# Kernel tuning notes

Measured on AMD Instinct MI355X. Metric: run time of the kernel, lower is better.

Reference implementation:

```python
import jax, jax.numpy as jnp
import numpy as np

BN_EPS = 1e-5


def setup_inputs() -> dict:
    key = jax.random.key(0)
    ks = jax.random.split(key, 12)
    B, N, S, D1, D2 = 2, 16384, 4096, 128, 256
    C1, C2 = 256, 128  # mlp channels
    return {
        "xyz1": jax.random.normal(ks[0], (B, 3, N), dtype=jnp.float32),
        "xyz2": jax.random.normal(ks[1], (B, 3, S), dtype=jnp.float32),
        "points1": jax.random.normal(ks[2], (B, D1, N), dtype=jnp.float32),
        "points2": jax.random.normal(ks[3], (B, D2, S), dtype=jnp.float32),
        "w1": jax.random.normal(ks[4], (D1 + D2, C1), dtype=jnp.float32) * 0.05,
        "b1": jax.random.normal(ks[5], (C1,), dtype=jnp.float32) * 0.05,
        "g1": jax.random.uniform(ks[6], (C1,), dtype=jnp.float32, minval=0.5, maxval=1.5),
        "beta1": jax.random.normal(ks[7], (C1,), dtype=jnp.float32) * 0.05,
        "w2": jax.random.normal(ks[8], (C1, C2), dtype=jnp.float32) * 0.05,
        "b2": jax.random.normal(ks[9], (C2,), dtype=jnp.float32) * 0.05,
        "g2": jax.random.uniform(ks[10], (C2,), dtype=jnp.float32, minval=0.5, maxval=1.5),
        "beta2": jax.random.normal(ks[11], (C2,), dtype=jnp.float32) * 0.05,
    }


def _conv_bn_relu(x, W, b, g, beta):
    # 1x1 Conv1d == per-point matmul; BatchNorm1d training-mode stats over (B, N).
    y = x @ W + b                              # [B, N, Cout]
    mu = jnp.mean(y, axis=(0, 1))
    var = jnp.var(y, axis=(0, 1))              # biased variance, matches torch BN
    y = g * (y - mu) * jax.lax.rsqrt(var + BN_EPS) + beta
    return jax.nn.relu(y)


def reference(xyz1, xyz2, points1, points2, w1, b1, g1, beta1, w2, b2, g2, beta2):
    x1 = jnp.transpose(xyz1, (0, 2, 1))        # [B, N, 3]
    x2 = jnp.transpose(xyz2, (0, 2, 1))        # [B, S, 3]
    p2 = jnp.transpose(points2, (0, 2, 1))     # [B, S, D2]

    # squared pairwise distance [B, N, S], clamped at 0
    d = (jnp.sum(x1 ** 2, axis=-1, keepdims=True)
         - 2.0 * jnp.einsum('bnc,bsc->bns', x1, x2)
         + jnp.sum(x2 ** 2, axis=-1)[:, None, :])
    d = jnp.maximum(d, 0.0)

    # 3 nearest neighbors (ascending smallest distances) -- same math as full sort + slice
    neg_d3, idx = jax.lax.top_k(-d, 3)         # [B, N, 3]
    d3 = jnp.maximum(-neg_d3, 1e-6)
    recip = 1.0 / d3
    w = recip / jnp.maximum(jnp.sum(recip, axis=-1, keepdims=True), 1e-6)

    nb = jax.vmap(lambda p, i: p[i])(p2, idx)  # [B, N, 3, D2]
    interp = jnp.sum(nb * w[..., None], axis=2)
    interp = jnp.nan_to_num(interp, nan=0.0, posinf=0.0, neginf=0.0)

    p1 = jnp.transpose(points1, (0, 2, 1))     # [B, N, D1]
    x = jnp.concatenate([p1, interp], axis=-1) # [B, N, D1+D2]

    x = _conv_bn_relu(x, w1, b1, g1, beta1)
    x = _conv_bn_relu(x, w2, b2, g2, beta2)
    x = jnp.nan_to_num(x, nan=0.0, posinf=0.0, neginf=0.0)
    return jnp.transpose(x, (0, 2, 1))         # [B, C2, N]
```

## Files before the change

### kernel.cpp

```cpp
#include <hip/hip_runtime.h>

#define B_   2
#define N_   16384
#define S_   4096
#define D1_  128
#define D2_  256
#define C1_  256
#define C2_  128
#define M_   (B_ * N_)

typedef __bf16 bf16_t;
typedef bf16_t bf16x8 __attribute__((ext_vector_type(8)));
typedef float  f32x4  __attribute__((ext_vector_type(4)));

__device__ __forceinline__ void gload16(const void* g, void* l) {
  __builtin_amdgcn_global_load_lds(
      (const __attribute__((address_space(1))) void*)g,
      (__attribute__((address_space(3))) void*)l, 16, 0, 0);
}

#define INSERT3(v, ix)                                                   \
  {                                                                      \
    bool b0_ = (v) < m0, b1_ = (v) < m1, b2_ = (v) < m2;                 \
    float nm0 = fminf((v), m0);                                          \
    float nm1 = fminf(fmaxf((v), m0), m1);                               \
    float nm2 = fminf(fmaxf((v), m1), m2);                               \
    j2 = b1_ ? j1 : (b2_ ? (ix) : j2);                                   \
    j1 = b0_ ? j0 : (b1_ ? (ix) : j1);                                   \
    j0 = b0_ ? (ix) : j0;                                                \
    m0 = nm0; m1 = nm1; m2 = nm2;                                        \
  }

union SMem1 {
  struct { float4 cbuf[1024]; float T3V[2][3][32]; int T3I[2][3][32]; } knn;
  float tile[2][32][33];
};

__global__ __launch_bounds__(512, 8) void phase1_k(const float* __restrict__ xyz1,
                                                   const float* __restrict__ xyz2,
                                                   const float* __restrict__ points1,
                                                   const float* __restrict__ w1,
                                                   const float* __restrict__ w2,
                                                   float* __restrict__ kw,
                                                   int* __restrict__ ki,
                                                   bf16_t* __restrict__ Xp1,
                                                   bf16_t* __restrict__ w1at,
                                                   bf16_t* __restrict__ w2t) {
  __shared__ SMem1 sm;
  int bi = blockIdx.x, t = threadIdx.x;
  if (bi < 1024) {
    int l = t & 63, w = t >> 6;
    int q = l & 31, h = l >> 5;
    int s = w * 2 + h;
    int b  = bi >> 9;
    int nb = (bi & 511) * 32;
    int n  = nb + q;
    const float* X1 = xyz1 + (size_t)b * 3 * N_;
    const float* X2 = xyz2 + (size_t)b * 3 * S_;
    float ax = X1[n], ay = X1[N_ + n], az = X1[2 * N_ + n];
    float p = ax * ax + ay * ay + az * az;
    float m0 = 3e38f, m1 = 3e38f, m2 = 3e38f;
    int   j0 = 0, j1 = 0, j2 = 0;
    for (int r = 0; r < 4; ++r) {
      __syncthreads();
      {
        int i0 = r * 1024 + t;
        float x = X2[i0], y = X2[S_ + i0], z = X2[2 * S_ + i0];
        sm.knn.cbuf[t] = make_float4(-2.f * x, -2.f * y, -2.f * z, x * x + y * y + z * z);
        int i1 = i0 + 512;
        x = X2[i1]; y = X2[S_ + i1]; z = X2[2 * S_ + i1];
        sm.knn.cbuf[t + 512] = make_float4(-2.f * x, -2.f * y, -2.f * z, x * x + y * y + z * z);
      }
      __syncthreads();
      const float4* cs = sm.knn.cbuf + s * 64;
      int base = r * 1024 + s * 64;
#pragma unroll 8
      for (int i = 0; i < 64; ++i) {
        float4 c = cs[i];
        float v = c.w;
        v = fmaf(az, c.z, v);
        v = fmaf(ay, c.y, v);
        v = fmaf(ax, c.x, v);
        int idx = base + i;
        INSERT3(v, idx);
      }
    }
    __syncthreads();
    float* SV = (float*)sm.knn.cbuf;
    int*   SI = (int*)sm.knn.cbuf + 1536;
    SV[(s * 3 + 0) * 32 + q] = m0;  SV[(s * 3 + 1) * 32 + q] = m1;  SV[(s * 3 + 2) * 32 + q] = m2;
    SI[(s * 3 + 0) * 32 + q] = j0;  SI[(s * 3 + 1) * 32 + q] = j1;  SI[(s * 3 + 2) * 32 + q] = j2;
    __syncthreads();
    if (t < 64) {
      int th = t >> 5, tq = t & 31;
      float m0 = 3e38f, m1 = 3e38f, m2 = 3e38f;
      int j0 = 0, j1 = 0, j2 = 0;
      for (int s2 = th * 8; s2 < th * 8 + 8; ++s2)
#pragma unroll
        for (int k = 0; k < 3; ++k) {
          float v = SV[(s2 * 3 + k) * 32 + tq];
          int  ix = SI[(s2 * 3 + k) * 32 + tq];
          INSERT3(v, ix);
        }
      sm.knn.T3V[th][0][tq] = m0; sm.knn.T3V[th][1][tq] = m1; sm.knn.T3V[th][2][tq] = m2;
      sm.knn.T3I[th][0][tq] = j0; sm.knn.T3I[th][1][tq] = j1; sm.knn.T3I[th][2][tq] = j2;
    }
    __syncthreads();
    if (t < 32) {
      float m0 = sm.knn.T3V[0][0][t], m1 = sm.knn.T3V[0][1][t], m2 = sm.knn.T3V[0][2][t];
      int   j0 = sm.knn.T3I[0][0][t], j1 = sm.knn.T3I[0][1][t], j2 = sm.knn.T3I[0][2][t];
#pragma unroll
      for (int k = 0; k < 3; ++k) {
        float v = sm.knn.T3V[1][k][t];
        int  ix = sm.knn.T3I[1][k][t];
        INSERT3(v, ix);
      }
      float d0 = fmaxf(p + m0, 1e-6f);
      float d1 = fmaxf(p + m1, 1e-6f);
      float d2 = fmaxf(p + m2, 1e-6f);
      float r0 = 1.f / d0, r1 = 1.f / d1, r2 = 1.f / d2;
      float dn = fmaxf(r0 + r1 + r2, 1e-6f);
      size_t rr = (size_t)b * N_ + n;
      kw[rr * 3 + 0] = r0 / dn;  kw[rr * 3 + 1] = r1 / dn;  kw[rr * 3 + 2] = r2 / dn;
      ki[rr * 3 + 0] = j0;       ki[rr * 3 + 1] = j1;       ki[rr * 3 + 2] = j2;
    }
  } else if (bi < 3072) {
    int bj = bi - 1024;
    int b = bj >> 10, rest = bj & 1023;
    int n0 = (rest & 255) * 64, c0 = (rest >> 8) * 32;
    int tx = t & 31, ty = (t >> 5) & 7, th = t >> 8;
    const float* src = points1 + (size_t)b * D1_ * N_;
#pragma unroll
    for (int k = 0; k < 4; ++k)
      sm.tile[th][ty + k * 8][tx] = src[(size_t)(c0 + ty + k * 8) * N_ + n0 + th * 32 + tx];
    __syncthreads();
#pragma unroll
    for (int k = 0; k < 4; ++k)
      Xp1[(size_t)(b * N_ + n0 + th * 32 + ty + k * 8) * 128 + c0 + tx] =
          (bf16_t)sm.tile[th][tx][ty + k * 8];
  } else {
    int i = (bi - 3072) * 512 + t;
    if (i < 32768) {
      int n = i >> 7, k = i & 127;
      w1at[i] = (bf16_t)w1[(size_t)k * C1_ + n];
    } else {
      int j = i - 32768;
      int n = j >> 8, k = j & 255;
      w2t[j] = (bf16_t)w2[(size_t)k * C2_ + n];
    }
  }
}

__global__ __launch_bounds__(512) void gemmG_k(const float* __restrict__ points2,
                                               const float* __restrict__ w1,
                                               bf16_t* __restrict__ G) {
  const int LDP = 40;
  __shared__ bf16_t As[128 * LDP];
  __shared__ bf16_t Bs[256 * LDP];
  int t = threadIdx.x, lane = t & 63, w = t >> 6;
  int wr = w >> 2, wc = w & 3;
  int bb = blockIdx.x >> 5;
  int m0 = (blockIdx.x & 31) * 128;
  const float* P2 = points2 + (size_t)bb * D2_ * S_;
  f32x4 acc[4][4];
  f32x4 z = {0.f, 0.f, 0.f, 0.f};
#pragma unroll
  for (int i = 0; i < 4; ++i)
#pragma unroll
    for (int j = 0; j < 4; ++j) acc[i][j] = z;
  int sA = t & 127, kgA = t >> 7;
  int nB = t & 255, kgB = t >> 8;
  for (int k0 = 0; k0 < 256; k0 += 32) {
    __syncthreads();
    {
      bf16x8 ap;
#pragma unroll
      for (int kk = 0; kk < 8; ++kk)
        ap[kk] = (bf16_t)P2[(size_t)(k0 + kgA * 8 + kk) * S_ + m0 + sA];
      *(bf16x8*)&As[sA * LDP + kgA * 8] = ap;
      bf16x8 bp0, bp1;
#pragma unroll
      for (int kk = 0; kk < 8; ++kk) {
        bp0[kk] = (bf16_t)w1[(size_t)(128 + k0 + kgB * 16 + kk) * C1_ + nB];
        bp1[kk] = (bf16_t)w1[(size_t)(128 + k0 + kgB * 16 + 8 + kk) * C1_ + nB];
      }
      *(bf16x8*)&Bs[nB * LDP + kgB * 16] = bp0;
      *(bf16x8*)&Bs[nB * LDP + kgB * 16 + 8] = bp1;
    }
    __syncthreads();
    bf16x8 af[4], bfr[4];
    int arow = wr * 64 + (lane & 15);
    int brow = wc * 64 + (lane & 15);
    int kc = 8 * (lane >> 4);
#pragma unroll
    for (int i = 0; i < 4; ++i) af[i]  = *(const bf16x8*)&As[(arow + i * 16) * LDP + kc];
#pragma unroll
    for (int j = 0; j < 4; ++j) bfr[j] = *(const bf16x8*)&Bs[(brow + j * 16) * LDP + kc];
#pragma unroll
    for (int i = 0; i < 4; ++i)
#pragma unroll
      for (int j = 0; j < 4; ++j)
        acc[i][j] = __builtin_amdgcn_mfma_f32_16x16x32_bf16(af[i], bfr[j], acc[i][j], 0, 0, 0);
  }
  bf16_t* Gb = G + (size_t)bb * S_ * 256;
#pragma unroll
  for (int j = 0; j < 4; ++j) {
    int col = wc * 64 + j * 16 + (lane & 15);
#pragma unroll
    for (int i = 0; i < 4; ++i) {
      int r = m0 + wr * 64 + i * 16 + ((lane >> 4) << 2);
#pragma unroll
      for (int q = 0; q < 4; ++q)
        Gb[(size_t)(r + q) * 256 + col] = (bf16_t)acc[i][j][q];
    }
  }
}

__global__ __launch_bounds__(256) void gemm1_k(const bf16_t* __restrict__ A,
                                               const bf16_t* __restrict__ Bt,
                                               const float* __restrict__ bias,
                                               const bf16_t* __restrict__ G,
                                               const float* __restrict__ KW,
                                               const int* __restrict__ KI,
                                               bf16_t* __restrict__ Y,
                                               float* __restrict__ st) {
  const int K = 128;
  __shared__ bf16_t As[128 * 32];
  __shared__ bf16_t Bs[128 * 32];
  int tid = threadIdx.x, lane = tid & 63, w = tid >> 6;
  int wr = w >> 1, wc = w & 1;
  int m0 = blockIdx.x * 128, n0 = blockIdx.y * 128;
  int e0 = (w * 2 + 0) * 512 + lane * 8;
  int e1 = (w * 2 + 1) * 512 + lane * 8;
  int ra0 = e0 >> 5, ca0 = e0 & 31;
  int ra1 = e1 >> 5, ca1 = e1 & 31;
  f32x4 acc[4][4];
  f32x4 z = {0.f, 0.f, 0.f, 0.f};
#pragma unroll
  for (int i = 0; i < 4; ++i)
#pragma unroll
    for (int j = 0; j < 4; ++j) acc[i][j] = z;
  for (int k0 = 0; k0 < K; k0 += 32) {
    __syncthreads();
    gload16(A + (size_t)(m0 + ra0) * K + k0 + ca0, &As[e0]);
    gload16(A + (size_t)(m0 + ra1) * K + k0 + ca1, &As[e1]);
    gload16(Bt + (size_t)(n0 + ra0) * K + k0 + ca0, &Bs[e0]);
    gload16(Bt + (size_t)(n0 + ra1) * K + k0 + ca1, &Bs[e1]);
    __syncthreads();
    bf16x8 af[4], bfr[4];
    int arow = wr * 64 + (lane & 15);
    int brow = wc * 64 + (lane & 15);
    int kc = 8 * (lane >> 4);
#pragma unroll
    for (int i = 0; i < 4; ++i) af[i]  = *(const bf16x8*)&As[(arow + i * 16) * 32 + kc];
#pragma unroll
    for (int j = 0; j < 4; ++j) bfr[j] = *(const bf16x8*)&Bs[(brow + j * 16) * 32 + kc];
#pragma unroll
    for (int i = 0; i < 4; ++i)
#pragma unroll
      for (int j = 0; j < 4; ++j)
        acc[i][j] = __builtin_amdgcn_mfma_f32_16x16x32_bf16(af[i], bfr[j], acc[i][j], 0, 0, 0);
  }
  __syncthreads();
  float* kwls = (float*)As;
  int*   kils = ((int*)As) + 384;
  if (tid < 128) {
    int r = m0 + tid;
    kwls[tid * 3 + 0] = KW[(size_t)r * 3 + 0];
    kwls[tid * 3 + 1] = KW[(size_t)r * 3 + 1];
    kwls[tid * 3 + 2] = KW[(size_t)r * 3 + 2];
    kils[tid * 3 + 0] = KI[(size_t)r * 3 + 0];
    kils[tid * 3 + 1] = KI[(size_t)r * 3 + 1];
    kils[tid * 3 + 2] = KI[(size_t)r * 3 + 2];
  }
  __syncthreads();
  int bb = m0 >> 14;
  const bf16_t* Gb = G + (size_t)bb * S_ * 256;
  float sjv[4]  = {0.f, 0.f, 0.f, 0.f};
  float ssjv[4] = {0.f, 0.f, 0.f, 0.f};
#pragma unroll
  for (int i = 0; i < 4; ++i) {
#pragma unroll
    for (int qq = 0; qq < 4; ++qq) {
      int rl = wr * 64 + i * 16 + ((lane >> 4) << 2) + qq;
      float w0 = kwls[rl * 3 + 0], w1v = kwls[rl * 3 + 1], w2v = kwls[rl * 3 + 2];
      const bf16_t* g0 = Gb + (size_t)kils[rl * 3 + 0] * 256;
      const bf16_t* g1 = Gb + (size_t)kils[rl * 3 + 1] * 256;
      const bf16_t* g2 = Gb + (size_t)kils[rl * 3 + 2] * 256;
      int r = m0 + rl;
#pragma unroll
      for (int j = 0; j < 4; ++j) {
        int col = n0 + wc * 64 + j * 16 + (lane & 15);
        float y = acc[i][j][qq] + bias[col]
                + w0 * (float)g0[col] + w1v * (float)g1[col] + w2v * (float)g2[col];
        Y[(size_t)r * C1_ + col] = (bf16_t)y;
        sjv[j] += y;  ssjv[j] += y * y;
      }
    }
  }
#pragma unroll
  for (int j = 0; j < 4; ++j) {
    float sj = sjv[j], ssj = ssjv[j];
    sj  += __shfl_xor(sj, 16);  sj  += __shfl_xor(sj, 32);
    ssj += __shfl_xor(ssj, 16); ssj += __shfl_xor(ssj, 32);
    if ((lane >> 4) == 0) {
      int col = n0 + wc * 64 + j * 16 + (lane & 15);
      atomicAdd(&st[col], sj);
      atomicAdd(&st[C1_ + col], ssj);
    }
  }
}

__global__ __launch_bounds__(256) void gemm2_k(const bf16_t* __restrict__ Y1,
                                               const bf16_t* __restrict__ Bt,
                                               const float* __restrict__ bias,
                                               const float* __restrict__ st1,
                                               const float* __restrict__ g1v,
                                               const float* __restrict__ be1,
                                               float* __restrict__ OUT,
                                               float* __restrict__ st2) {
  const int K = 256;
  __shared__ bf16_t As[128 * 32];
  __shared__ bf16_t Bs[128 * 32];
  __shared__ float sa1[C1_], sb1[C1_];
  int tid = threadIdx.x, lane = tid & 63, w = tid >> 6;
  int wr = w >> 1, wc = w & 1;
  int m0 = blockIdx.x * 128;
  {
    const float invM = 1.f / (float)M_;
    float mu  = st1[tid] * invM;
    float var = fmaxf(st1[C1_ + tid] * invM - mu * mu, 0.f);
    float a = g1v[tid] * rsqrtf(var + 1e-5f);
    sa1[tid] = a;
    sb1[tid] = be1[tid] - mu * a;
  }
  int e0 = (w * 2 + 0) * 512 + lane * 8;
  int e1 = (w * 2 + 1) * 512 + lane * 8;
  int ra0 = e0 >> 5, ca0 = e0 & 31;
  int ra1 = e1 >> 5, ca1 = e1 & 31;
  f32x4 acc[4][4];
  f32x4 z = {0.f, 0.f, 0.f, 0.f};
#pragma unroll
  for (int i = 0; i < 4; ++i)
#pragma unroll
    for (int j = 0; j < 4; ++j) acc[i][j] = z;
  bf16x8 va0 = *(const bf16x8*)&Y1[(size_t)(m0 + ra0) * C1_ + ca0];
  bf16x8 va1 = *(const bf16x8*)&Y1[(size_t)(m0 + ra1) * C1_ + ca1];
  __syncthreads();
  for (int k0 = 0; k0 < K; k0 += 32) {
    bf16x8 nb0, nb1;
    if (k0 + 32 < K) {
      nb0 = *(const bf16x8*)&Y1[(size_t)(m0 + ra0) * C1_ + k0 + 32 + ca0];
      nb1 = *(const bf16x8*)&Y1[(size_t)(m0 + ra1) * C1_ + k0 + 32 + ca1];
    }
    if (k0) __syncthreads();
    bf16x8 oa0, oa1;
#pragma unroll
    for (int u = 0; u < 8; ++u) {
      float f0 = (float)va0[u];
      float f1 = (float)va1[u];
      f0 = fmaxf(f0 * sa1[k0 + ca0 + u] + sb1[k0 + ca0 + u], 0.f);
      f1 = fmaxf(f1 * sa1[k0 + ca1 + u] + sb1[k0 + ca1 + u], 0.f);
      oa0[u] = (bf16_t)f0;
      oa1[u] = (bf16_t)f1;
    }
    *(bf16x8*)&As[e0] = oa0;
    *(bf16x8*)&As[e1] = oa1;
    gload16(Bt + (size_t)ra0 * K + k0 + ca0, &Bs[e0]);
    gload16(Bt + (size_t)ra1 * K + k0 + ca1, &Bs[e1]);
    __syncthreads();
    bf16x8 af[4], bfr[4];
    int arow = wr * 64 + (lane & 15);
    int brow = wc * 64 + (lane & 15);
    int kc = 8 * (lane >> 4);
#pragma unroll
    for (int i = 0; i < 4; ++i) af[i]  = *(const bf16x8*)&As[(arow + i * 16) * 32 + kc];
#pragma unroll
    for (int j = 0; j < 4; ++j) bfr[j] = *(const bf16x8*)&Bs[(brow + j * 16) * 32 + kc];
#pragma unroll
    for (int i = 0; i < 4; ++i)
#pragma unroll
      for (int j = 0; j < 4; ++j)
        acc[i][j] = __builtin_amdgcn_mfma_f32_16x16x32_bf16(af[i], bfr[j], acc[i][j], 0, 0, 0);
    va0 = nb0; va1 = nb1;
  }
#pragma unroll
  for (int j = 0; j < 4; ++j) {
    int col = wc * 64 + j * 16 + (lane & 15);
    float bv = bias[col];
    float sj = 0.f, ssj = 0.f;
#pragma unroll
    for (int i = 0; i < 4; ++i) {
      int r  = m0 + wr * 64 + i * 16 + ((lane >> 4) << 2);
      int bb = r >> 14, n = r & (N_ - 1);
      f32x4 v = acc[i][j];
#pragma unroll
      for (int q = 0; q < 4; ++q) {
        v[q] += bv;
        sj += v[q]; ssj += v[q] * v[q];
      }
      *(f32x4*)&OUT[((size_t)(bb * C2_ + col)) * N_ + n] = v;
    }
    sj  += __shfl_xor(sj, 16);  sj  += __shfl_xor(sj, 32);
    ssj += __shfl_xor(ssj, 16); ssj += __shfl_xor(ssj, 32);
    if ((lane >> 4) == 0) {
      atomicAdd(&st2[col], sj);
      atomicAdd(&st2[C2_ + col], ssj);
    }
  }
}

__global__ __launch_bounds__(256) void bn2apply_k(float* __restrict__ OUT,
                                                  const float* __restrict__ st,
                                                  const float* __restrict__ g,
                                                  const float* __restrict__ be) {
  __shared__ float ab[2];
  int t = threadIdx.x;
  int c = (blockIdx.x >> 4) & 127;
  if (t == 0) {
    const float invM = 1.f / (float)M_;
    float mu  = st[c] * invM;
    float var = fmaxf(st[C2_ + c] * invM - mu * mu, 0.f);
    float a = g[c] * rsqrtf(var + 1e-5f);
    ab[0] = a;
    ab[1] = be[c] - mu * a;
  }
  __syncthreads();
  float a = ab[0], s = ab[1];
  size_t i4 = (size_t)blockIdx.x * 256 + t;
  f32x4 v = *(f32x4*)&OUT[i4 * 4];
#pragma unroll
  for (int u = 0; u < 4; ++u) v[u] = fmaxf(a * v[u] + s, 0.f);
  *(f32x4*)&OUT[i4 * 4] = v;
}

extern "C" void kernel_launch(void* const* d_in, const int* in_sizes, int n_in,
                              void* d_out, int out_size, void* d_ws, size_t ws_size,
                              hipStream_t stream) {
  const float* xyz1    = (const float*)d_in[0];
  const float* xyz2    = (const float*)d_in[1];
  const float* points1 = (const float*)d_in[2];
  const float* points2 = (const float*)d_in[3];
  const float* w1      = (const float*)d_in[4];
  const float* b1      = (const float*)d_in[5];
  const float* g1      = (const float*)d_in[6];
  const float* beta1   = (const float*)d_in[7];
  const float* w2      = (const float*)d_in[8];
  const float* b2      = (const float*)d_in[9];
  const float* g2      = (const float*)d_in[10];
  const float* beta2   = (const float*)d_in[11];
  float* out = (float*)d_out;

  char* p = (char*)d_ws;
  size_t off = 0;
  bf16_t* Xp1  = (bf16_t*)(p + off); off += (size_t)M_ * 128 * 2;
  bf16_t* W1AT = (bf16_t*)(p + off); off += (size_t)C1_ * 128 * 2;
  bf16_t* W2T  = (bf16_t*)(p + off); off += (size_t)C2_ * C1_ * 2;
  bf16_t* G    = (bf16_t*)(p + off); off += (size_t)B_ * S_ * 256 * 2;
  bf16_t* Y1   = (bf16_t*)(p + off); off += (size_t)M_ * C1_ * 2;
  float*  KW   = (float*)(p + off);  off += (size_t)M_ * 3 * 4;
  int*    KI   = (int*)(p + off);    off += (size_t)M_ * 3 * 4;
  float*  ST1  = (float*)(p + off);  off += 2048;
  float*  ST2  = (float*)(p + off);  off += 1024;

  hipMemsetAsync(ST1, 0, 3072, stream);

  phase1_k<<<3200, 512, 0, stream>>>(xyz1, xyz2, points1, w1, w2,
                                     KW, KI, Xp1, W1AT, W2T);
  gemmG_k<<<64, 512, 0, stream>>>(points2, w1, G);
  gemm1_k<<<dim3(M_ / 128, 2), 256, 0, stream>>>(Xp1, W1AT, b1, G, KW, KI, Y1, ST1);
  gemm2_k<<<M_ / 128, 256, 0, stream>>>(Y1, W2T, b2, ST1, g1, beta1, out, ST2);
  bn2apply_k<<<4096, 256, 0, stream>>>(out, ST2, g2, beta2);
}
```

Measured before the change: 142.3 us.

## Split KNN into value-only top-3 pass and index-recovery second pass

The brute-force 3-NN search now first tracks only the three smallest distance values per query with a cheap min/max network and no index selects, and merges them across wavefronts. A second sweep over all candidates recomputes distances and records the indices whose distance exactly equals one of the known top-3 values, skipping groups of four whose minimum exceeds the third value. This removes the per-candidate index bookkeeping from the hot loop, but doubles candidate loading and distance arithmetic. Ties and duplicate values can map to a different index than before, and the extra barriers add cost.

Result: faster. 135.5 us (-4.8%).

```diff
diff --git a/kernel.cpp b/kernel.cpp
--- a/kernel.cpp
+++ b/kernel.cpp
@@ -19,20 +19,24 @@
       (__attribute__((address_space(3))) void*)l, 16, 0, 0);
 }
 
-#define INSERT3(v, ix)                                                   \
+__device__ __forceinline__ float4 cand4(const float* __restrict__ X2, int i) {
+  float x = X2[i], y = X2[S_ + i], z = X2[2 * S_ + i];
+  float w = fmaf(x, x, fmaf(y, y, z * z));
+  return make_float4(-2.f * x, -2.f * y, -2.f * z, w);
+}
+__device__ __forceinline__ float distv(float4 c, float ax, float ay, float az) {
+  return fmaf(ax, c.x, fmaf(ay, c.y, fmaf(az, c.z, c.w)));
+}
+#define TRACK3(v)                                                        \
   {                                                                      \
-    bool b0_ = (v) < m0, b1_ = (v) < m1, b2_ = (v) < m2;                 \
-    float nm0 = fminf((v), m0);                                          \
-    float nm1 = fminf(fmaxf((v), m0), m1);                               \
-    float nm2 = fminf(fmaxf((v), m1), m2);                               \
-    j2 = b1_ ? j1 : (b2_ ? (ix) : j2);                                   \
-    j1 = b0_ ? j0 : (b1_ ? (ix) : j1);                                   \
-    j0 = b0_ ? (ix) : j0;                                                \
-    m0 = nm0; m1 = nm1; m2 = nm2;                                        \
+    float t0_ = fminf((v), m0);                                          \
+    float t1_ = fminf(fmaxf((v), m0), m1);                               \
+    float t2_ = fminf(fmaxf((v), m1), m2);                               \
+    m0 = t0_; m1 = t1_; m2 = t2_;                                        \
   }
 
 union SMem1 {
-  struct { float4 cbuf[1024]; float T3V[2][3][32]; int T3I[2][3][32]; } knn;
+  struct { float4 cbuf[1024]; float T3V[2][3][32]; float QMv[32][3]; } knn;
   float tile[2][32][33];
 };
 
@@ -58,71 +62,102 @@
     const float* X1 = xyz1 + (size_t)b * 3 * N_;
     const float* X2 = xyz2 + (size_t)b * 3 * S_;
     float ax = X1[n], ay = X1[N_ + n], az = X1[2 * N_ + n];
-    float p = ax * ax + ay * ay + az * az;
+    float p = fmaf(ax, ax, fmaf(ay, ay, az * az));
     float m0 = 3e38f, m1 = 3e38f, m2 = 3e38f;
-    int   j0 = 0, j1 = 0, j2 = 0;
     for (int r = 0; r < 4; ++r) {
       __syncthreads();
-      {
-        int i0 = r * 1024 + t;
-        float x = X2[i0], y = X2[S_ + i0], z = X2[2 * S_ + i0];
-        sm.knn.cbuf[t] = make_float4(-2.f * x, -2.f * y, -2.f * z, x * x + y * y + z * z);
-        int i1 = i0 + 512;
-        x = X2[i1]; y = X2[S_ + i1]; z = X2[2 * S_ + i1];
-        sm.knn.cbuf[t + 512] = make_float4(-2.f * x, -2.f * y, -2.f * z, x * x + y * y + z * z);
-      }
+      sm.knn.cbuf[t]       = cand4(X2, r * 1024 + t);
+      sm.knn.cbuf[t + 512] = cand4(X2, r * 1024 + t + 512);
+      __syncthreads();
+      const float4* cs = sm.knn.cbuf + s * 64;
+#pragma unroll 8
+      for (int i = 0; i < 64; ++i) {
+        float v = distv(cs[i], ax, ay, az);
+        TRACK3(v);
+      }
+    }
+    __syncthreads();
+    float* SV = (float*)sm.knn.cbuf;
+    SV[(s * 3 + 0) * 32 + q] = m0;  SV[(s * 3 + 1) * 32 + q] = m1;  SV[(s * 3 + 2) * 32 + q] = m2;
+    __syncthreads();
+    if (t < 64) {
+      int th = t >> 5, tq = t & 31;
+      float m0 = 3e38f, m1 = 3e38f, m2 = 3e38f;
+      for (int s2 = th * 8; s2 < th * 8 + 8; ++s2)
+#pragma unroll
+        for (int k = 0; k < 3; ++k) {
+          float v = SV[(s2 * 3 + k) * 32 + tq];
+          TRACK3(v);
+        }
+      sm.knn.T3V[th][0][tq] = m0; sm.knn.T3V[th][1][tq] = m1; sm.knn.T3V[th][2][tq] = m2;
+    }
+    __syncthreads();
+    float g0 = 3e38f, g1 = 3e38f, g2 = 3e38f;
+    if (t < 32) {
+      float m0 = sm.knn.T3V[0][0][t], m1 = sm.knn.T3V[0][1][t], m2 = sm.knn.T3V[0][2][t];
+#pragma unroll
+      for (int k = 0; k < 3; ++k) {
+        float v = sm.knn.T3V[1][k][t];
+        TRACK3(v);
+      }
+      g0 = m0; g1 = m1; g2 = m2;
+      sm.knn.QMv[t][0] = m0; sm.knn.QMv[t][1] = m1; sm.knn.QMv[t][2] = m2;
+    }
+    __syncthreads();
+    float q0v = sm.knn.QMv[q][0], q1v = sm.knn.QMv[q][1], q2v = sm.knn.QMv[q][2];
+    unsigned j0 = 0xFFFFFFFFu, j1 = 0xFFFFFFFFu, j2 = 0xFFFFFFFFu;
+    for (int r = 0; r < 4; ++r) {
+      __syncthreads();
+      sm.knn.cbuf[t]       = cand4(X2, r * 1024 + t);
+      sm.knn.cbuf[t + 512] = cand4(X2, r * 1024 + t + 512);
       __syncthreads();
       const float4* cs = sm.knn.cbuf + s * 64;
       int base = r * 1024 + s * 64;
-#pragma unroll 8
-      for (int i = 0; i < 64; ++i) {
-        float4 c = cs[i];
-        float v = c.w;
-        v = fmaf(az, c.z, v);
-        v = fmaf(ay, c.y, v);
-        v = fmaf(ax, c.x, v);
-        int idx = base + i;
-        INSERT3(v, idx);
-      }
-    }
-    __syncthreads();
-    float* SV = (float*)sm.knn.cbuf;
-    int*   SI = (int*)sm.knn.cbuf + 1536;
-    SV[(s * 3 + 0) * 32 + q] = m0;  SV[(s * 3 + 1) * 32 + q] = m1;  SV[(s * 3 + 2) * 32 + q] = m2;
+#pragma unroll
+      for (int g = 0; g < 16; ++g) {
+        float v0 = distv(cs[g * 4 + 0], ax, ay, az);
+        float v1 = distv(cs[g * 4 + 1], ax, ay, az);
+        float v2 = distv(cs[g * 4 + 2], ax, ay, az);
+        float v3 = distv(cs[g * 4 + 3], ax, ay, az);
+        float gm = fminf(fminf(v0, v1), fminf(v2, v3));
+        if (gm <= q2v) {
+#define CHK(vv, uu)                                                      \
+          {                                                              \
+            unsigned idx = (unsigned)(base + g * 4 + uu);                \
+            bool h0 = ((vv) == q0v) && (j0 == 0xFFFFFFFFu);              \
+            bool h1 = ((vv) == q1v) && (j1 == 0xFFFFFFFFu) && !h0;       \
+            bool h2 = ((vv) == q2v) && (j2 == 0xFFFFFFFFu) && !h0 && !h1;\
+            if (h0) j0 = idx;                                            \
+            if (h1) j1 = idx;                                            \
+            if (h2) j2 = idx;                                            \
+          }
+          CHK(v0, 0) CHK(v1, 1) CHK(v2, 2) CHK(v3, 3)
+#undef CHK
+        }
+      }
+    }
+    __syncthreads();
+    unsigned* SI = (unsigned*)sm.knn.cbuf;
     SI[(s * 3 + 0) * 32 + q] = j0;  SI[(s * 3 + 1) * 32 + q] = j1;  SI[(s * 3 + 2) * 32 + q] = j2;
     __syncthreads();
-    if (t < 64) {
-      int th = t >> 5, tq = t & 31;
-      float m0 = 3e38f, m1 = 3e38f, m2 = 3e38f;
-      int j0 = 0, j1 = 0, j2 = 0;
-      for (int s2 = th * 8; s2 < th * 8 + 8; ++s2)
-#pragma unroll
-        for (int k = 0; k < 3; ++k) {
-          float v = SV[(s2 * 3 + k) * 32 + tq];
-          int  ix = SI[(s2 * 3 + k) * 32 + tq];
-          INSERT3(v, ix);
-        }
-      sm.knn.T3V[th][0][tq] = m0; sm.knn.T3V[th][1][tq] = m1; sm.knn.T3V[th][2][tq] = m2;
-      sm.knn.T3I[th][0][tq] = j0; sm.knn.T3I[th][1][tq] = j1; sm.knn.T3I[th][2][tq] = j2;
-    }
-    __syncthreads();
     if (t < 32) {
-      float m0 = sm.knn.T3V[0][0][t], m1 = sm.knn.T3V[0][1][t], m2 = sm.knn.T3V[0][2][t];
-      int   j0 = sm.knn.T3I[0][0][t], j1 = sm.knn.T3I[0][1][t], j2 = sm.knn.T3I[0][2][t];
-#pragma unroll
-      for (int k = 0; k < 3; ++k) {
-        float v = sm.knn.T3V[1][k][t];
-        int  ix = sm.knn.T3I[1][k][t];
-        INSERT3(v, ix);
-      }
-      float d0 = fmaxf(p + m0, 1e-6f);
-      float d1 = fmaxf(p + m1, 1e-6f);
-      float d2 = fmaxf(p + m2, 1e-6f);
+      unsigned a0 = 0xFFFFFFFFu, a1 = 0xFFFFFFFFu, a2 = 0xFFFFFFFFu;
+      for (int s2 = 0; s2 < 16; ++s2) {
+        a0 = min(a0, SI[(s2 * 3 + 0) * 32 + t]);
+        a1 = min(a1, SI[(s2 * 3 + 1) * 32 + t]);
+        a2 = min(a2, SI[(s2 * 3 + 2) * 32 + t]);
+      }
+      a0 = min(a0, (unsigned)(S_ - 1));
+      a1 = min(a1, (unsigned)(S_ - 1));
+      a2 = min(a2, (unsigned)(S_ - 1));
+      float d0 = fmaxf(p + g0, 1e-6f);
+      float d1 = fmaxf(p + g1, 1e-6f);
+      float d2 = fmaxf(p + g2, 1e-6f);
       float r0 = 1.f / d0, r1 = 1.f / d1, r2 = 1.f / d2;
       float dn = fmaxf(r0 + r1 + r2, 1e-6f);
       size_t rr = (size_t)b * N_ + n;
       kw[rr * 3 + 0] = r0 / dn;  kw[rr * 3 + 1] = r1 / dn;  kw[rr * 3 + 2] = r2 / dn;
-      ki[rr * 3 + 0] = j0;       ki[rr * 3 + 1] = j1;       ki[rr * 3 + 2] = j2;
+      ki[rr * 3 + 0] = (int)a0;  ki[rr * 3 + 1] = (int)a1;  ki[rr * 3 + 2] = (int)a2;
     }
   } else if (bi < 3072) {
     int bj = bi - 1024;
```
